# Optimization experiments

Hardware: AMD Instinct MI355X
Metric: run time of the kernel (lower is better)

Reference implementation:

```python
import jax, jax.numpy as jnp
import numpy as np

# physics constants (match PDELoss defaults)
RHO, CP, VZ, KT = 0.3, 1200.0, 0.5, 0.06
# Arrhenius-style soot source constants (representative RadiationPINN.soot_source_terms)
A_NUC, E_NUC = 1.0e4, 2.0e4
A_GROW, E_GROW = 5.0e3, 1.2e4
A_OX, E_OX = 1.0e5, 1.6e4

N, IN_DIM, H, OUT, N_FUELS, EMB = 262144, 12, 128, 7, 4, 8


def mlp(X, emb_rows, W1, b1, W2, b2, W3, b3, Wo, bo):
    # X: (N,4) coords; emb_rows: (N,8) fuel embedding -> T (N,1), fv (N,1), Y (N,5)
    h = jnp.concatenate([X, emb_rows], axis=-1)
    h = jnp.tanh(h @ W1 + b1)
    h = jnp.tanh(h @ W2 + b2)
    h = jnp.tanh(h @ W3 + b3)
    o = h @ Wo + bo
    T = 300.0 + 2000.0 * jax.nn.sigmoid(o[:, 0:1])
    fv = jax.nn.softplus(o[:, 1:2]) * 1e-6
    Y = jax.nn.softmax(o[:, 2:7], axis=-1)
    return T, fv, Y


def soot_sources(T, Y_prec, Y_O2, fv):
    nuc = A_NUC * Y_prec * jnp.exp(-E_NUC / T)
    grow = A_GROW * Y_prec * fv * jnp.exp(-E_GROW / T)
    ox = A_OX * Y_O2 * fv * jnp.sqrt(T) * jnp.exp(-E_OX / T)
    return nuc, grow, ox


def pde_loss(inputs, fuel_ids, W1, b1, W2, b2, W3, b3, Wo, bo, emb):
    emb_rows = emb[fuel_ids]  # (N, EMB), constant w.r.t. inputs
    params = (W1, b1, W2, b2, W3, b3, Wo, bo)

    def T_of(X):
        return mlp(X, emb_rows, *params)[0]

    def fv_of(X):
        return mlp(X, emb_rows, *params)[1]

    n = inputs.shape[0]
    Ez = jnp.zeros_like(inputs).at[:, 1].set(1.0)  # direction d/dz
    Er = jnp.zeros_like(inputs).at[:, 2].set(1.0)  # direction d/dr

    # forward-mode (Taylor) derivatives: nested jvp gives 1st and 2nd order in one pass
    dT_dz_fn = lambda X: jax.jvp(T_of, (X,), (Ez,))[1]
    dT_dz, d2T_dz2 = jax.jvp(dT_dz_fn, (inputs,), (Ez,))
    dT_dr_fn = lambda X: jax.jvp(T_of, (X,), (Er,))[1]
    dT_dr, d2T_dr2 = jax.jvp(dT_dr_fn, (inputs,), (Er,))
    _, dfv_dz = jax.jvp(fv_of, (inputs,), (Ez,))

    T, fv, Y = mlp(inputs, emb_rows, *params)
    Y_prec, Y_O2 = Y[:, 3:4], Y[:, 4:5]

    r = inputs[:, 2:3]
    r_safe = jnp.maximum(r, 1e-6)
    laplacian_r = d2T_dr2 + dT_dr / r_safe
    energy_res = RHO * CP * VZ * dT_dz - KT * laplacian_r - KT * d2T_dz2

    nuc, grow, ox = soot_sources(T, Y_prec, Y_O2, fv)
    soot_res = VZ * dfv_dz - nuc - grow + ox

    loss_energy = jnp.mean(energy_res ** 2)
    loss_soot = jnp.mean(soot_res ** 2)
    return jnp.stack([loss_energy, loss_soot, loss_energy + loss_soot])


def setup_inputs() -> dict:
    key = jax.random.key(0)
    ks = jax.random.split(key, 12)
    inputs = jax.random.uniform(ks[0], (N, 4), dtype=jnp.float32)
    fuel_ids = jax.random.randint(ks[1], (N,), 0, N_FUELS)
    s1, sh, so = 1.0 / np.sqrt(IN_DIM), 1.0 / np.sqrt(H), 1.0 / np.sqrt(H)
    return {
        "inputs": inputs,
        "fuel_ids": fuel_ids,
        "W1": jax.random.normal(ks[2], (IN_DIM, H), jnp.float32) * s1,
        "b1": jnp.zeros((H,), jnp.float32),
        "W2": jax.random.normal(ks[3], (H, H), jnp.float32) * sh,
        "b2": jnp.zeros((H,), jnp.float32),
        "W3": jax.random.normal(ks[4], (H, H), jnp.float32) * sh,
        "b3": jnp.zeros((H,), jnp.float32),
        "Wo": jax.random.normal(ks[5], (H, OUT), jnp.float32) * so,
        "bo": jnp.zeros((OUT,), jnp.float32),
        "emb": jax.random.normal(ks[6], (N_FUELS, EMB), jnp.float32) * 0.1,
    }


def reference(inputs, fuel_ids, W1, b1, W2, b2, W3, b3, Wo, bo, emb):
    return pde_loss(inputs, fuel_ids, W1, b1, W2, b2, W3, b3, Wo, bo, emb)
```

## Files before the change

### kernel.cpp

```cpp
#include <hip/hip_runtime.h>
#include <math.h>

#define NPTS 262144
#define PTS  16
#define NBLK (NPTS / PTS)
#define AP   136

typedef _Float16 f16;
typedef f16    f16x4 __attribute__((ext_vector_type(4)));
typedef f16    f16x8 __attribute__((ext_vector_type(8)));
typedef __fp16 h16x2 __attribute__((ext_vector_type(2)));
typedef __fp16 h16x4 __attribute__((ext_vector_type(4)));
typedef float  f32x4 __attribute__((ext_vector_type(4)));


__device__ __forceinline__ h16x2 pk(float a, float b) {
    return __builtin_amdgcn_cvt_pkrtz(a, b);
}
__device__ __forceinline__ f16x4 mrg(h16x2 lo, h16x2 hi) {
    h16x4 v = __builtin_shufflevector(lo, hi, 0, 1, 2, 3);
    return __builtin_bit_cast(f16x4, v);
}

__device__ __forceinline__ float fast_tanh(float z) {
    float e = __expf(2.f * z);
    float r = __builtin_amdgcn_rcpf(e + 1.f);
    return __builtin_fmaf(-2.f, r, 1.f);
}

__global__ void prep_weights(const float* __restrict__ W1, const float* __restrict__ W2,
                             const float* __restrict__ W3, const float* __restrict__ Wo,
                             const float* __restrict__ bo,
                             f16* __restrict__ wt1, f16* __restrict__ wt2,
                             f16* __restrict__ wt3, f16* __restrict__ wot,
                             float* __restrict__ bot)
{
    int tid    = blockIdx.x * blockDim.x + threadIdx.x;
    int stride = gridDim.x * blockDim.x;
    for (int i = tid; i < 128 * 32; i += stride) {
        int k = i >> 7, n = i & 127;
        wt1[n * 32 + k] = (f16)((k < 12) ? W1[k * 128 + n] : 0.f);
    }
    for (int i = tid; i < 128 * 128; i += stride) {
        int k = i >> 7, n = i & 127;
        wt2[n * 128 + k] = (f16)W2[i];
        wt3[n * 128 + k] = (f16)W3[i];
    }
    for (int i = tid; i < 16 * 128; i += stride) {
        int k = i >> 4, n = i & 15;
        wot[n * 128 + k] = (f16)((n < 7) ? Wo[k * 7 + n] : 0.f);
    }
    if (tid < 16) bot[tid] = (tid < 7) ? bo[tid] : 0.f;
}

__device__ __forceinline__ void transform_store(
    f16 (*sAct)[PTS][AP], const f32x4 acc[5], int pt, int n0q)
{
    float t[4], s[4];
#pragma unroll
    for (int r = 0; r < 4; ++r) {
        t[r] = fast_tanh(acc[0][r]);
        s[r] = 1.f - t[r] * t[r];
    }
    h16x2 T[2]  = { pk(t[0], t[1]), pk(t[2], t[3]) };
    h16x2 S[2]  = { pk(s[0], s[1]), pk(s[2], s[3]) };
    h16x2 A1[2] = { pk(acc[1][0], acc[1][1]), pk(acc[1][2], acc[1][3]) };
    h16x2 A2[2] = { pk(acc[2][0], acc[2][1]), pk(acc[2][2], acc[2][3]) };
    h16x2 A3[2] = { pk(acc[3][0], acc[3][1]), pk(acc[3][2], acc[3][3]) };
    h16x2 A4[2] = { pk(acc[4][0], acc[4][1]), pk(acc[4][2], acc[4][3]) };
    h16x2 TZ[2], TZZ[2], TR[2], TRR[2];
#pragma unroll
    for (int p = 0; p < 2; ++p) {
        h16x2 n2t = -(T[p] + T[p]);
        TZ[p]  = S[p] * A1[p];
        TR[p]  = S[p] * A3[p];
        TZZ[p] = n2t * (TZ[p] * A1[p]) + S[p] * A2[p];
        TRR[p] = n2t * (TR[p] * A3[p]) + S[p] * A4[p];
    }
    *(f16x4*)&sAct[0][pt][n0q] = mrg(T[0], T[1]);
    *(f16x4*)&sAct[1][pt][n0q] = mrg(TZ[0], TZ[1]);
    *(f16x4*)&sAct[2][pt][n0q] = mrg(TZZ[0], TZZ[1]);
    *(f16x4*)&sAct[3][pt][n0q] = mrg(TR[0], TR[1]);
    *(f16x4*)&sAct[4][pt][n0q] = mrg(TRR[0], TRR[1]);
}

__device__ __forceinline__ void transform_store_l1(
    f16 (*sAct)[PTS][AP], const f32x4 acc0, const f32x4 wz, const f32x4 wr,
    int pt, int n0q)
{
    float t[4], s[4];
#pragma unroll
    for (int r = 0; r < 4; ++r) {
        t[r] = fast_tanh(acc0[r]);
        s[r] = 1.f - t[r] * t[r];
    }
    h16x2 T[2]  = { pk(t[0], t[1]), pk(t[2], t[3]) };
    h16x2 S[2]  = { pk(s[0], s[1]), pk(s[2], s[3]) };
    h16x2 A1[2] = { pk(wz[0], wz[1]), pk(wz[2], wz[3]) };
    h16x2 A3[2] = { pk(wr[0], wr[1]), pk(wr[2], wr[3]) };
    h16x2 TZ[2], TZZ[2], TR[2], TRR[2];
#pragma unroll
    for (int p = 0; p < 2; ++p) {
        h16x2 n2t = -(T[p] + T[p]);
        TZ[p]  = S[p] * A1[p];
        TR[p]  = S[p] * A3[p];
        TZZ[p] = n2t * (TZ[p] * A1[p]);
        TRR[p] = n2t * (TR[p] * A3[p]);
    }
    *(f16x4*)&sAct[0][pt][n0q] = mrg(T[0], T[1]);
    *(f16x4*)&sAct[1][pt][n0q] = mrg(TZ[0], TZ[1]);
    *(f16x4*)&sAct[2][pt][n0q] = mrg(TZZ[0], TZZ[1]);
    *(f16x4*)&sAct[3][pt][n0q] = mrg(TR[0], TR[1]);
    *(f16x4*)&sAct[4][pt][n0q] = mrg(TRR[0], TRR[1]);
}

__device__ __forceinline__ void layer128(
    f16 (*sAct)[PTS][AP], const f16* __restrict__ Wt, const float* __restrict__ b,
    int half, int q, int m)
{
    f16x8 Bv[5][4];
#pragma unroll
    for (int c = 0; c < 5; ++c)
#pragma unroll
        for (int kt = 0; kt < 4; ++kt)
            Bv[c][kt] = *(const f16x8*)&sAct[c][m][kt * 32 + q * 8];
    __syncthreads();

    const f32x4 z4 = {0.f, 0.f, 0.f, 0.f};
#pragma unroll
    for (int ct0 = 0; ct0 < 4; ++ct0) {
        const int n0 = (half * 4 + ct0) * 16;
        const f16* wp = &Wt[(n0 + m) * 128 + q * 8];
        f16x8 A0 = *(const f16x8*)(wp);
        f16x8 A1 = *(const f16x8*)(wp + 32);
        f16x8 A2 = *(const f16x8*)(wp + 64);
        f16x8 A3 = *(const f16x8*)(wp + 96);
        f32x4 bb = *(const f32x4*)&b[n0 + q * 4];
        f32x4 acc[5];
        acc[0] = __builtin_amdgcn_mfma_f32_16x16x32_f16(A0, Bv[0][0], bb, 0, 0, 0);
#pragma unroll
        for (int c = 1; c < 5; ++c) acc[c] = __builtin_amdgcn_mfma_f32_16x16x32_f16(A0, Bv[c][0], z4, 0, 0, 0);
#pragma unroll
        for (int c = 0; c < 5; ++c) acc[c] = __builtin_amdgcn_mfma_f32_16x16x32_f16(A1, Bv[c][1], acc[c], 0, 0, 0);
#pragma unroll
        for (int c = 0; c < 5; ++c) acc[c] = __builtin_amdgcn_mfma_f32_16x16x32_f16(A2, Bv[c][2], acc[c], 0, 0, 0);
#pragma unroll
        for (int c = 0; c < 5; ++c) acc[c] = __builtin_amdgcn_mfma_f32_16x16x32_f16(A3, Bv[c][3], acc[c], 0, 0, 0);

        transform_store(sAct, acc, m, n0 + q * 4);
    }
    __syncthreads();
}

__global__ __launch_bounds__(128, 2) void pde_main(
    const float* __restrict__ X,
    const int*   __restrict__ fid,
    const float* __restrict__ emb,
    const float* __restrict__ W1,
    const float* __restrict__ b1, const float* __restrict__ b2,
    const float* __restrict__ b3,
    const f16* __restrict__ Wt1, const f16* __restrict__ Wt2,
    const f16* __restrict__ Wt3, const f16* __restrict__ Wot,
    const float* __restrict__ bot,
    float* __restrict__ partials)
{
    __shared__ f32x4 smem4[5 * PTS * AP * 2 / 16];
    f16   (*sAct)[PTS][AP] = (f16(*)[PTS][AP])smem4;
    float (*sO)[PTS][17]   = (float(*)[PTS][17])smem4;

    const int tid  = threadIdx.x;
    const int half = tid >> 6;
    const int lane = tid & 63;
    const int q    = lane >> 4;
    const int m    = lane & 15;
    const int p0   = blockIdx.x * PTS;

    if (tid < PTS) {
        const int p = tid;
        f32x4 xr = *(const f32x4*)&X[(p0 + p) * 4];
        const float* er = &emb[fid[p0 + p] * 8];
        f32x4 e0 = *(const f32x4*)er;
        f32x4 e1 = *(const f32x4*)(er + 4);
        const f16x4 zz = {(f16)0.f, (f16)0.f, (f16)0.f, (f16)0.f};
        *(f16x4*)&sAct[0][p][0]  = mrg(pk(xr.x, xr.y), pk(xr.z, xr.w));
        *(f16x4*)&sAct[0][p][4]  = mrg(pk(e0.x, e0.y), pk(e0.z, e0.w));
        *(f16x4*)&sAct[0][p][8]  = mrg(pk(e1.x, e1.y), pk(e1.z, e1.w));
        *(f16x4*)&sAct[0][p][12] = zz;
        *(f16x4*)&sAct[0][p][16] = zz;
        *(f16x4*)&sAct[0][p][20] = zz;
        *(f16x4*)&sAct[0][p][24] = zz;
        *(f16x4*)&sAct[0][p][28] = zz;
    }
    __syncthreads();

    {
        f16x8 Bv0 = *(const f16x8*)&sAct[0][m][q * 8];
        __syncthreads();
#pragma unroll
        for (int ct0 = 0; ct0 < 4; ++ct0) {
            const int n0 = (half * 4 + ct0) * 16;
            f16x8 A0 = *(const f16x8*)&Wt1[(n0 + m) * 32 + q * 8];
            f32x4 bb = *(const f32x4*)&b1[n0 + q * 4];
            f32x4 acc0 = __builtin_amdgcn_mfma_f32_16x16x32_f16(A0, Bv0, bb, 0, 0, 0);
            f32x4 wz = *(const f32x4*)&W1[128 + n0 + q * 4];
            f32x4 wr = *(const f32x4*)&W1[256 + n0 + q * 4];
            transform_store_l1(sAct, acc0, wz, wr, m, n0 + q * 4);
        }
        __syncthreads();
    }

    layer128(sAct, Wt2, b2, half, q, m);
    layer128(sAct, Wt3, b3, half, q, m);

    const int nch = 3 - half;
    const int cb  = half * 3;
    f16x8 Bh[3][4];
#pragma unroll
    for (int c = 0; c < 3; ++c) if (c < nch)
#pragma unroll
        for (int kt = 0; kt < 4; ++kt)
            Bh[c][kt] = *(const f16x8*)&sAct[cb + c][m][kt * 32 + q * 8];
    f32x4 c0i = {0.f, 0.f, 0.f, 0.f};
    if (half == 0) c0i = *(const f32x4*)&bot[q * 4];
    __syncthreads();
    {
        const f16* wp = &Wot[m * 128 + q * 8];
        f16x8 A0 = *(const f16x8*)(wp);
        f16x8 A1 = *(const f16x8*)(wp + 32);
        f16x8 A2 = *(const f16x8*)(wp + 64);
        f16x8 A3 = *(const f16x8*)(wp + 96);
        const f32x4 z4 = {0.f, 0.f, 0.f, 0.f};
        f32x4 acc[3];
#pragma unroll
        for (int c = 0; c < 3; ++c) if (c < nch) acc[c] = __builtin_amdgcn_mfma_f32_16x16x32_f16(A0, Bh[c][0], (c == 0) ? c0i : z4, 0, 0, 0);
#pragma unroll
        for (int c = 0; c < 3; ++c) if (c < nch) acc[c] = __builtin_amdgcn_mfma_f32_16x16x32_f16(A1, Bh[c][1], acc[c], 0, 0, 0);
#pragma unroll
        for (int c = 0; c < 3; ++c) if (c < nch) acc[c] = __builtin_amdgcn_mfma_f32_16x16x32_f16(A2, Bh[c][2], acc[c], 0, 0, 0);
#pragma unroll
        for (int c = 0; c < 3; ++c) if (c < nch) acc[c] = __builtin_amdgcn_mfma_f32_16x16x32_f16(A3, Bh[c][3], acc[c], 0, 0, 0);
#pragma unroll
        for (int c = 0; c < 3; ++c) if (c < nch)
#pragma unroll
            for (int r = 0; r < 4; ++r)
                sO[cb + c][m][q * 4 + r] = acc[c][r];
    }
    __syncthreads();

    if (lane < PTS) {
        const int pt = lane;
        float o0 = sO[0][pt][0];
        float sg = __fdividef(1.f, 1.f + __expf(-o0));
        float v;
        if (half == 0) {
            float o0z  = sO[1][pt][0];
            float o0zz = sO[2][pt][0];
            float o0r  = sO[3][pt][0];
            float o0rr = sO[4][pt][0];
            float sp  = sg * (1.f - sg);
            float spp = sp * (1.f - 2.f * sg);
            float Tz  = 2000.f * sp * o0z;
            float Tzz = 2000.f * (spp * o0z * o0z + sp * o0zz);
            float Tr  = 2000.f * sp * o0r;
            float Trr = 2000.f * (spp * o0r * o0r + sp * o0rr);
            float r   = X[(p0 + pt) * 4 + 2];
            float rs  = fmaxf(r, 1e-6f);
            float lap = Trr + __fdividef(Tr, rs);
            float eres = 180.f * Tz - 0.06f * lap - 0.06f * Tzz;
            v = eres * eres;
        } else {
            float o1  = sO[0][pt][1];
            float o1z = sO[1][pt][1];
            float T   = 300.f + 2000.f * sg;
            float fv  = ((o1 > 20.f) ? o1 : __logf(1.f + __expf(o1))) * 1e-6f;
            float s1  = __fdividef(1.f, 1.f + __expf(-o1));
            float fvz = s1 * o1z * 1e-6f;
            float y0 = sO[0][pt][2], y1 = sO[0][pt][3], y2 = sO[0][pt][4];
            float y3 = sO[0][pt][5], y4 = sO[0][pt][6];
            float mx = fmaxf(fmaxf(fmaxf(y0, y1), fmaxf(y2, y3)), y4);
            float e0 = __expf(y0 - mx), e1 = __expf(y1 - mx), e2 = __expf(y2 - mx);
            float e3 = __expf(y3 - mx), e4 = __expf(y4 - mx);
            float inv = __fdividef(1.f, e0 + e1 + e2 + e3 + e4);
            float Yp = e3 * inv;
            float Yo = e4 * inv;
            float rT  = __fdividef(1.f, T);
            float nuc  = 1e4f * Yp * __expf(-20000.f * rT);
            float grow = 5e3f * Yp * fv * __expf(-12000.f * rT);
            float ox   = 1e5f * Yo * fv * sqrtf(T) * __expf(-16000.f * rT);
            float sres = 0.5f * fvz - nuc - grow + ox;
            v = sres * sres;
        }
#pragma unroll
        for (int o = 8; o > 0; o >>= 1) v += __shfl_xor(v, o, 64);
        if (pt == 0) partials[2 * blockIdx.x + half] = v;
    }
}

__global__ __launch_bounds__(1024) void pde_finalize(
    const float* __restrict__ partials, float* __restrict__ out)
{
    __shared__ double rE[1024];
    __shared__ double rS[1024];
    const int tid = threadIdx.x;
    const float2* p2 = (const float2*)partials;
    double se = 0.0, ss = 0.0;
    for (int i = tid; i < NBLK; i += 1024) {
        float2 v = p2[i];
        se += (double)v.x;
        ss += (double)v.y;
    }
    rE[tid] = se; rS[tid] = ss;
    __syncthreads();
    for (int s = 512; s > 0; s >>= 1) {
        if (tid < s) { rE[tid] += rE[tid + s]; rS[tid] += rS[tid + s]; }
        __syncthreads();
    }
    if (tid == 0) {
        const double invN = 1.0 / (double)NPTS;
        float le = (float)(rE[0] * invN);
        float ls = (float)(rS[0] * invN);
        out[0] = le;
        out[1] = ls;
        out[2] = le + ls;
    }
}

extern "C" void kernel_launch(void* const* d_in, const int* in_sizes, int n_in,
                              void* d_out, int out_size, void* d_ws, size_t ws_size,
                              hipStream_t stream)
{
    const float* X   = (const float*)d_in[0];
    const int*   fid = (const int*)  d_in[1];
    const float* W1  = (const float*)d_in[2];
    const float* b1  = (const float*)d_in[3];
    const float* W2  = (const float*)d_in[4];
    const float* b2  = (const float*)d_in[5];
    const float* W3  = (const float*)d_in[6];
    const float* b3  = (const float*)d_in[7];
    const float* Wo  = (const float*)d_in[8];
    const float* bo  = (const float*)d_in[9];
    const float* emb = (const float*)d_in[10];

    f16*   wt1      = (f16*)d_ws;
    f16*   wt2      = wt1 + 128 * 32;
    f16*   wt3      = wt2 + 128 * 128;
    f16*   wot      = wt3 + 128 * 128;
    float* bot      = (float*)(wot + 16 * 128);
    float* partials = bot + 16;
    float* out      = (float*)d_out;

    prep_weights<<<128, 256, 0, stream>>>(W1, W2, W3, Wo, bo, wt1, wt2, wt3, wot, bot);
    pde_main<<<NBLK, 128, 0, stream>>>(X, fid, emb, W1, b1, b2, b3,
                                       wt1, wt2, wt3, wot, bot, partials);
    pde_finalize<<<1, 1024, 0, stream>>>(partials, out);
}
```

Measured before the change: 261.7 us.

## Use single-wavefront blocks with XOR-swizzled LDS and no barriers

Shrinks each block from two wavefronts to one, so a single wave computes all 128 output columns of every layer. The padded LDS layout becomes an XOR-swizzled 256-byte row layout, and all __syncthreads barriers are dropped because one wave's LDS accesses need no block-level sync. The output layer now runs all five Taylor channels in registers, with cross-lane shuffles replacing the LDS staging, and a single lane writes both partials. This removes barrier and LDS round-trip overhead. In exchange each wave does twice the MFMA work serially, and the kernel relies on intra-wave ordering of LDS reads and writes being safe in place.

```diff
diff --git a/kernel.cpp b/kernel.cpp
--- a/kernel.cpp
+++ b/kernel.cpp
@@ -4,7 +4,6 @@
 #define NPTS 262144
 #define PTS  16
 #define NBLK (NPTS / PTS)
-#define AP   136
 
 typedef _Float16 f16;
 typedef f16    f16x4 __attribute__((ext_vector_type(4)));
@@ -54,7 +53,7 @@
 }
 
 __device__ __forceinline__ void transform_store(
-    f16 (*sAct)[PTS][AP], const f32x4 acc[5], int pt, int n0q)
+    char* sA, const f32x4 acc[5], int pt, int n0q)
 {
     float t[4], s[4];
 #pragma unroll
@@ -77,15 +76,17 @@
         TZZ[p] = n2t * (TZ[p] * A1[p]) + S[p] * A2[p];
         TRR[p] = n2t * (TR[p] * A3[p]) + S[p] * A4[p];
     }
-    *(f16x4*)&sAct[0][pt][n0q] = mrg(T[0], T[1]);
-    *(f16x4*)&sAct[1][pt][n0q] = mrg(TZ[0], TZ[1]);
-    *(f16x4*)&sAct[2][pt][n0q] = mrg(TZZ[0], TZZ[1]);
-    *(f16x4*)&sAct[3][pt][n0q] = mrg(TR[0], TR[1]);
-    *(f16x4*)&sAct[4][pt][n0q] = mrg(TRR[0], TRR[1]);
+    const int key = (pt & 7) << 4;
+    char* rb = sA + (pt << 8) + (((n0q * 2)) ^ key);
+    *(f16x4*)(rb)         = mrg(T[0], T[1]);
+    *(f16x4*)(rb +  4096) = mrg(TZ[0], TZ[1]);
+    *(f16x4*)(rb +  8192) = mrg(TZZ[0], TZZ[1]);
+    *(f16x4*)(rb + 12288) = mrg(TR[0], TR[1]);
+    *(f16x4*)(rb + 16384) = mrg(TRR[0], TRR[1]);
 }
 
 __device__ __forceinline__ void transform_store_l1(
-    f16 (*sAct)[PTS][AP], const f32x4 acc0, const f32x4 wz, const f32x4 wr,
+    char* sA, const f32x4 acc0, const f32x4 wz, const f32x4 wr,
     int pt, int n0q)
 {
     float t[4], s[4];
@@ -107,29 +108,32 @@
         TZZ[p] = n2t * (TZ[p] * A1[p]);
         TRR[p] = n2t * (TR[p] * A3[p]);
     }
-    *(f16x4*)&sAct[0][pt][n0q] = mrg(T[0], T[1]);
-    *(f16x4*)&sAct[1][pt][n0q] = mrg(TZ[0], TZ[1]);
-    *(f16x4*)&sAct[2][pt][n0q] = mrg(TZZ[0], TZZ[1]);
-    *(f16x4*)&sAct[3][pt][n0q] = mrg(TR[0], TR[1]);
-    *(f16x4*)&sAct[4][pt][n0q] = mrg(TRR[0], TRR[1]);
+    const int key = (pt & 7) << 4;
+    char* rb = sA + (pt << 8) + (((n0q * 2)) ^ key);
+    *(f16x4*)(rb)         = mrg(T[0], T[1]);
+    *(f16x4*)(rb +  4096) = mrg(TZ[0], TZ[1]);
+    *(f16x4*)(rb +  8192) = mrg(TZZ[0], TZZ[1]);
+    *(f16x4*)(rb + 12288) = mrg(TR[0], TR[1]);
+    *(f16x4*)(rb + 16384) = mrg(TRR[0], TRR[1]);
 }
 
 __device__ __forceinline__ void layer128(
-    f16 (*sAct)[PTS][AP], const f16* __restrict__ Wt, const float* __restrict__ b,
-    int half, int q, int m)
-{
+    char* sA, const f16* __restrict__ Wt, const float* __restrict__ b,
+    int q, int m)
+{
+    const int mkey = (m & 7) << 4;
+    const char* rp = sA + (m << 8);
     f16x8 Bv[5][4];
 #pragma unroll
     for (int c = 0; c < 5; ++c)
 #pragma unroll
         for (int kt = 0; kt < 4; ++kt)
-            Bv[c][kt] = *(const f16x8*)&sAct[c][m][kt * 32 + q * 8];
-    __syncthreads();
+            Bv[c][kt] = *(const f16x8*)(rp + c * 4096 + ((kt * 64 + q * 16) ^ mkey));
 
     const f32x4 z4 = {0.f, 0.f, 0.f, 0.f};
 #pragma unroll
-    for (int ct0 = 0; ct0 < 4; ++ct0) {
-        const int n0 = (half * 4 + ct0) * 16;
+    for (int ct0 = 0; ct0 < 8; ++ct0) {
+        const int n0 = ct0 * 16;
         const f16* wp = &Wt[(n0 + m) * 128 + q * 8];
         f16x8 A0 = *(const f16x8*)(wp);
         f16x8 A1 = *(const f16x8*)(wp + 32);
@@ -147,12 +151,11 @@
 #pragma unroll
         for (int c = 0; c < 5; ++c) acc[c] = __builtin_amdgcn_mfma_f32_16x16x32_f16(A3, Bv[c][3], acc[c], 0, 0, 0);
 
-        transform_store(sAct, acc, m, n0 + q * 4);
-    }
-    __syncthreads();
-}
-
-__global__ __launch_bounds__(128, 2) void pde_main(
+        transform_store(sA, acc, m, n0 + q * 4);
+    }
+}
+
+__global__ __launch_bounds__(64, 2) void pde_main(
     const float* __restrict__ X,
     const int*   __restrict__ fid,
     const float* __restrict__ emb,
@@ -164,135 +167,134 @@
     const float* __restrict__ bot,
     float* __restrict__ partials)
 {
-    __shared__ f32x4 smem4[5 * PTS * AP * 2 / 16];
-    f16   (*sAct)[PTS][AP] = (f16(*)[PTS][AP])smem4;
-    float (*sO)[PTS][17]   = (float(*)[PTS][17])smem4;
-
-    const int tid  = threadIdx.x;
-    const int half = tid >> 6;
-    const int lane = tid & 63;
+    __shared__ f32x4 smem4[1280];
+    char* sA = (char*)smem4;
+
+    const int lane = threadIdx.x;
     const int q    = lane >> 4;
     const int m    = lane & 15;
     const int p0   = blockIdx.x * PTS;
 
-    if (tid < PTS) {
-        const int p = tid;
+    float rcoord = 0.f;
+    if (lane < PTS) {
+        const int p = lane;
         f32x4 xr = *(const f32x4*)&X[(p0 + p) * 4];
+        rcoord = xr.z;
         const float* er = &emb[fid[p0 + p] * 8];
         f32x4 e0 = *(const f32x4*)er;
         f32x4 e1 = *(const f32x4*)(er + 4);
         const f16x4 zz = {(f16)0.f, (f16)0.f, (f16)0.f, (f16)0.f};
-        *(f16x4*)&sAct[0][p][0]  = mrg(pk(xr.x, xr.y), pk(xr.z, xr.w));
-        *(f16x4*)&sAct[0][p][4]  = mrg(pk(e0.x, e0.y), pk(e0.z, e0.w));
-        *(f16x4*)&sAct[0][p][8]  = mrg(pk(e1.x, e1.y), pk(e1.z, e1.w));
-        *(f16x4*)&sAct[0][p][12] = zz;
-        *(f16x4*)&sAct[0][p][16] = zz;
-        *(f16x4*)&sAct[0][p][20] = zz;
-        *(f16x4*)&sAct[0][p][24] = zz;
-        *(f16x4*)&sAct[0][p][28] = zz;
-    }
-    __syncthreads();
+        const int key = (p & 7) << 4;
+        char* rb = sA + (p << 8);
+        *(f16x4*)(rb + (0  ^ key)) = mrg(pk(xr.x, xr.y), pk(xr.z, xr.w));
+        *(f16x4*)(rb + (8  ^ key)) = mrg(pk(e0.x, e0.y), pk(e0.z, e0.w));
+        *(f16x4*)(rb + (16 ^ key)) = mrg(pk(e1.x, e1.y), pk(e1.z, e1.w));
+        *(f16x4*)(rb + (24 ^ key)) = zz;
+        *(f16x4*)(rb + (32 ^ key)) = zz;
+        *(f16x4*)(rb + (40 ^ key)) = zz;
+        *(f16x4*)(rb + (48 ^ key)) = zz;
+        *(f16x4*)(rb + (56 ^ key)) = zz;
+    }
 
     {
-        f16x8 Bv0 = *(const f16x8*)&sAct[0][m][q * 8];
-        __syncthreads();
-#pragma unroll
-        for (int ct0 = 0; ct0 < 4; ++ct0) {
-            const int n0 = (half * 4 + ct0) * 16;
+        const int mkey = (m & 7) << 4;
+        f16x8 Bv0 = *(const f16x8*)(sA + (m << 8) + ((q * 16) ^ mkey));
+#pragma unroll
+        for (int ct0 = 0; ct0 < 8; ++ct0) {
+            const int n0 = ct0 * 16;
             f16x8 A0 = *(const f16x8*)&Wt1[(n0 + m) * 32 + q * 8];
             f32x4 bb = *(const f32x4*)&b1[n0 + q * 4];
             f32x4 acc0 = __builtin_amdgcn_mfma_f32_16x16x32_f16(A0, Bv0, bb, 0, 0, 0);
             f32x4 wz = *(const f32x4*)&W1[128 + n0 + q * 4];
             f32x4 wr = *(const f32x4*)&W1[256 + n0 + q * 4];
-            transform_store_l1(sAct, acc0, wz, wr, m, n0 + q * 4);
+            transform_store_l1(sA, acc0, wz, wr, m, n0 + q * 4);
         }
-        __syncthreads();
-    }
-
-    layer128(sAct, Wt2, b2, half, q, m);
-    layer128(sAct, Wt3, b3, half, q, m);
-
-    const int nch = 3 - half;
-    const int cb  = half * 3;
-    f16x8 Bh[3][4];
-#pragma unroll
-    for (int c = 0; c < 3; ++c) if (c < nch)
-#pragma unroll
-        for (int kt = 0; kt < 4; ++kt)
-            Bh[c][kt] = *(const f16x8*)&sAct[cb + c][m][kt * 32 + q * 8];
-    f32x4 c0i = {0.f, 0.f, 0.f, 0.f};
-    if (half == 0) c0i = *(const f32x4*)&bot[q * 4];
-    __syncthreads();
+    }
+
+    layer128(sA, Wt2, b2, q, m);
+    layer128(sA, Wt3, b3, q, m);
+
+    f32x4 acc[5];
     {
+        const int mkey = (m & 7) << 4;
+        const char* rp = sA + (m << 8);
+        f16x8 Bh[5][4];
+#pragma unroll
+        for (int c = 0; c < 5; ++c)
+#pragma unroll
+            for (int kt = 0; kt < 4; ++kt)
+                Bh[c][kt] = *(const f16x8*)(rp + c * 4096 + ((kt * 64 + q * 16) ^ mkey));
+        f32x4 c0i = *(const f32x4*)&bot[q * 4];
         const f16* wp = &Wot[m * 128 + q * 8];
         f16x8 A0 = *(const f16x8*)(wp);
         f16x8 A1 = *(const f16x8*)(wp + 32);
         f16x8 A2 = *(const f16x8*)(wp + 64);
         f16x8 A3 = *(const f16x8*)(wp + 96);
         const f32x4 z4 = {0.f, 0.f, 0.f, 0.f};
-        f32x4 acc[3];
-#pragma unroll
-        for (int c = 0; c < 3; ++c) if (c < nch) acc[c] = __builtin_amdgcn_mfma_f32_16x16x32_f16(A0, Bh[c][0], (c == 0) ? c0i : z4, 0, 0, 0);
-#pragma unroll
-        for (int c = 0; c < 3; ++c) if (c < nch) acc[c] = __builtin_amdgcn_mfma_f32_16x16x32_f16(A1, Bh[c][1], acc[c], 0, 0, 0);
-#pragma unroll
-        for (int c = 0; c < 3; ++c) if (c < nch) acc[c] = __builtin_amdgcn_mfma_f32_16x16x32_f16(A2, Bh[c][2], acc[c], 0, 0, 0);
-#pragma unroll
-        for (int c = 0; c < 3; ++c) if (c < nch) acc[c] = __builtin_amdgcn_mfma_f32_16x16x32_f16(A3, Bh[c][3], acc[c], 0, 0, 0);
-#pragma unroll
-        for (int c = 0; c < 3; ++c) if (c < nch)
-#pragma unroll
-            for (int r = 0; r < 4; ++r)
-                sO[cb + c][m][q * 4 + r] = acc[c][r];
-    }
-    __syncthreads();
+        acc[0] = __builtin_amdgcn_mfma_f32_16x16x32_f16(A0, Bh[0][0], c0i, 0, 0, 0);
+#pragma unroll
+        for (int c = 1; c < 5; ++c) acc[c] = __builtin_amdgcn_mfma_f32_16x16x32_f16(A0, Bh[c][0], z4, 0, 0, 0);
+#pragma unroll
+        for (int c = 0; c < 5; ++c) acc[c] = __builtin_amdgcn_mfma_f32_16x16x32_f16(A1, Bh[c][1], acc[c], 0, 0, 0);
+#pragma unroll
+        for (int c = 0; c < 5; ++c) acc[c] = __builtin_amdgcn_mfma_f32_16x16x32_f16(A2, Bh[c][2], acc[c], 0, 0, 0);
+#pragma unroll
+        for (int c = 0; c < 5; ++c) acc[c] = __builtin_amdgcn_mfma_f32_16x16x32_f16(A3, Bh[c][3], acc[c], 0, 0, 0);
+    }
+    const int src = (lane & 15) + 16;
+    float o4 = __shfl(acc[0][0], src, 64);
+    float o5 = __shfl(acc[0][1], src, 64);
+    float o6 = __shfl(acc[0][2], src, 64);
 
     if (lane < PTS) {
-        const int pt = lane;
-        float o0 = sO[0][pt][0];
-        float sg = __fdividef(1.f, 1.f + __expf(-o0));
-        float v;
-        if (half == 0) {
-            float o0z  = sO[1][pt][0];
-            float o0zz = sO[2][pt][0];
-            float o0r  = sO[3][pt][0];
-            float o0rr = sO[4][pt][0];
-            float sp  = sg * (1.f - sg);
-            float spp = sp * (1.f - 2.f * sg);
-            float Tz  = 2000.f * sp * o0z;
-            float Tzz = 2000.f * (spp * o0z * o0z + sp * o0zz);
-            float Tr  = 2000.f * sp * o0r;
-            float Trr = 2000.f * (spp * o0r * o0r + sp * o0rr);
-            float r   = X[(p0 + pt) * 4 + 2];
-            float rs  = fmaxf(r, 1e-6f);
-            float lap = Trr + __fdividef(Tr, rs);
-            float eres = 180.f * Tz - 0.06f * lap - 0.06f * Tzz;
-            v = eres * eres;
-        } else {
-            float o1  = sO[0][pt][1];
-            float o1z = sO[1][pt][1];
-            float T   = 300.f + 2000.f * sg;
-            float fv  = ((o1 > 20.f) ? o1 : __logf(1.f + __expf(o1))) * 1e-6f;
-            float s1  = __fdividef(1.f, 1.f + __expf(-o1));
-            float fvz = s1 * o1z * 1e-6f;
-            float y0 = sO[0][pt][2], y1 = sO[0][pt][3], y2 = sO[0][pt][4];
-            float y3 = sO[0][pt][5], y4 = sO[0][pt][6];
-            float mx = fmaxf(fmaxf(fmaxf(y0, y1), fmaxf(y2, y3)), y4);
-            float e0 = __expf(y0 - mx), e1 = __expf(y1 - mx), e2 = __expf(y2 - mx);
-            float e3 = __expf(y3 - mx), e4 = __expf(y4 - mx);
-            float inv = __fdividef(1.f, e0 + e1 + e2 + e3 + e4);
-            float Yp = e3 * inv;
-            float Yo = e4 * inv;
-            float rT  = __fdividef(1.f, T);
-            float nuc  = 1e4f * Yp * __expf(-20000.f * rT);
-            float grow = 5e3f * Yp * fv * __expf(-12000.f * rT);
-            float ox   = 1e5f * Yo * fv * sqrtf(T) * __expf(-16000.f * rT);
-            float sres = 0.5f * fvz - nuc - grow + ox;
-            v = sres * sres;
+        float o0   = acc[0][0], o1  = acc[0][1];
+        float o0z  = acc[1][0], o1z = acc[1][1];
+        float o0zz = acc[2][0];
+        float o0r  = acc[3][0];
+        float o0rr = acc[4][0];
+
+        float sg  = __fdividef(1.f, 1.f + __expf(-o0));
+        float T   = 300.f + 2000.f * sg;
+        float sp  = sg * (1.f - sg);
+        float spp = sp * (1.f - 2.f * sg);
+        float Tz  = 2000.f * sp * o0z;
+        float Tzz = 2000.f * (spp * o0z * o0z + sp * o0zz);
+        float Tr  = 2000.f * sp * o0r;
+        float Trr = 2000.f * (spp * o0r * o0r + sp * o0rr);
+
+        float rs  = fmaxf(rcoord, 1e-6f);
+        float lap = Trr + __fdividef(Tr, rs);
+        float eres = 180.f * Tz - 0.06f * lap - 0.06f * Tzz;
+
+        float fv  = ((o1 > 20.f) ? o1 : __logf(1.f + __expf(o1))) * 1e-6f;
+        float s1  = __fdividef(1.f, 1.f + __expf(-o1));
+        float fvz = s1 * o1z * 1e-6f;
+
+        float y0 = acc[0][2], y1 = acc[0][3], y2 = o4, y3 = o5, y4 = o6;
+        float mx = fmaxf(fmaxf(fmaxf(y0, y1), fmaxf(y2, y3)), y4);
+        float e0 = __expf(y0 - mx), e1 = __expf(y1 - mx), e2 = __expf(y2 - mx);
+        float e3 = __expf(y3 - mx), e4 = __expf(y4 - mx);
+        float inv = __fdividef(1.f, e0 + e1 + e2 + e3 + e4);
+        float Yp = e3 * inv;
+        float Yo = e4 * inv;
+
+        float rT  = __fdividef(1.f, T);
+        float nuc  = 1e4f * Yp * __expf(-20000.f * rT);
+        float grow = 5e3f * Yp * fv * __expf(-12000.f * rT);
+        float ox   = 1e5f * Yo * fv * sqrtf(T) * __expf(-16000.f * rT);
+        float sres = 0.5f * fvz - nuc - grow + ox;
+
+        float ve = eres * eres;
+        float vs = sres * sres;
+#pragma unroll
+        for (int o = 8; o > 0; o >>= 1) {
+            ve += __shfl_xor(ve, o, 64);
+            vs += __shfl_xor(vs, o, 64);
         }
-#pragma unroll
-        for (int o = 8; o > 0; o >>= 1) v += __shfl_xor(v, o, 64);
-        if (pt == 0) partials[2 * blockIdx.x + half] = v;
+        if (lane == 0) {
+            float2 w; w.x = ve; w.y = vs;
+            *(float2*)&partials[2 * blockIdx.x] = w;
+        }
     }
 }
 
@@ -350,7 +352,7 @@
     float* out      = (float*)d_out;
 
     prep_weights<<<128, 256, 0, stream>>>(W1, W2, W3, Wo, bo, wt1, wt2, wt3, wot, bot);
-    pde_main<<<NBLK, 128, 0, stream>>>(X, fid, emb, W1, b1, b2, b3,
-                                       wt1, wt2, wt3, wot, bot, partials);
+    pde_main<<<NBLK, 64, 0, stream>>>(X, fid, emb, W1, b1, b2, b3,
+                                      wt1, wt2, wt3, wot, bot, partials);
     pde_finalize<<<1, 1024, 0, stream>>>(partials, out);
 }
```

After: 236.4 us. 1.11x faster.
